# Optimization experiments

Hardware: AMD Instinct MI355X
Metric: run time of the kernel (lower is better)

## Reference

```python
import jax, jax.numpy as jnp
import numpy as np

B, TOPN, OUT, PAD, IOU_TH, IM = 16, 4, 224, 224, 0.25, 448
HP = IM + 2 * PAD  # padded image side = 896

_ANCHOR_SETTINGS = (
    dict(stride=32, size=48, scale=[2 ** (1. / 3.), 2 ** (2. / 3.)], aspect_ratio=[0.667, 1, 1.5]),
    dict(stride=64, size=96, scale=[2 ** (1. / 3.), 2 ** (2. / 3.)], aspect_ratio=[0.667, 1, 1.5]),
    dict(stride=128, size=192, scale=[1, 2 ** (1. / 3.), 2 ** (2. / 3.)], aspect_ratio=[0.667, 1, 1.5]),
)

def _edge_anchors(input_shape=(IM, IM)):
    # NTS-Net generate_default_anchor_maps: per layer, loop scale then aspect,
    # each emitting an HxW map flattened row-major -> matches tidy conv channel-major flatten.
    out = []
    for a in _ANCHOR_SETTINGS:
        st = a['stride']
        H = int(np.ceil(input_shape[0] / st)); W = int(np.ceil(input_shape[1] / st))
        cy = np.broadcast_to((np.arange(H) * st + st / 2.)[:, None], (H, W))
        cx = np.broadcast_to((np.arange(W) * st + st / 2.)[None, :], (H, W))
        for sc in a['scale']:
            for ar in a['aspect_ratio']:
                h = a['size'] * sc / np.sqrt(ar); w = a['size'] * sc * np.sqrt(ar)
                out.append(np.stack([cy - h / 2., cx - w / 2., cy + h / 2., cx + w / 2.], -1).reshape(-1, 4))
    e = np.concatenate(out, 0)
    return (e + PAD).astype(np.int32)  # module does (edge_anchors + 224).astype(int)


def _conv(x, w, b, stride, pad):
    y = jax.lax.conv_general_dilated(x, w, (stride, stride), [(pad, pad), (pad, pad)],
                                     dimension_numbers=('NCHW', 'OIHW', 'NCHW'))
    return y + b[None, :, None, None]


def _proposal_scores(rpn, w1, b1, w2, b2, w3, b3, wt1, bt1, wt2, bt2, wt3, bt3):
    d1 = jax.nn.relu(_conv(rpn, w1, b1, 1, 1))   # [B,128,14,14]
    d2 = jax.nn.relu(_conv(d1, w2, b2, 2, 1))    # [B,128,7,7]
    d3 = jax.nn.relu(_conv(d2, w3, b3, 2, 1))    # [B,128,4,4]
    bsz = rpn.shape[0]
    t1 = _conv(d1, wt1, bt1, 1, 0).reshape(bsz, -1)  # [B,1176]
    t2 = _conv(d2, wt2, bt2, 1, 0).reshape(bsz, -1)  # [B,294]
    t3 = _conv(d3, wt3, bt3, 1, 0).reshape(bsz, -1)  # [B,144]
    return jnp.concatenate([t1, t2, t3], axis=1)     # [B,1614]


def _nms_topn(scores, boxes, areas):
    # greedy hard NMS, fixed TOPN picks, suppress iou >= IOU_TH (matches upstream hard_nms)
    def step(s, _):
        i = jnp.argmax(s)
        sb = boxes[i]
        iy = jnp.clip(jnp.minimum(boxes[:, 2], sb[2]) - jnp.maximum(boxes[:, 0], sb[0]), 0.)
        ix = jnp.clip(jnp.minimum(boxes[:, 3], sb[3]) - jnp.maximum(boxes[:, 1], sb[1]), 0.)
        inter = iy * ix
        iou = inter / (areas + areas[i] - inter)
        return jnp.where(iou >= IOU_TH, -jnp.inf, s), i
    _, idxs = jax.lax.scan(step, scores, None, length=TOPN)
    return idxs  # [TOPN] int


def _crop_resize(x, anchors, top_idx):
    # batched replacement of the per-(i,j) F.interpolate(x_pad[i,:,y0:y1,x0:x1], 224, bilinear, align_corners=True)
    x_pad = jnp.pad(x, ((0, 0), (0, 0), (PAD, PAD), (PAD, PAD)))
    xp = jnp.transpose(x_pad, (0, 2, 3, 1))            # [B,HP,HP,3]
    bxs = anchors[top_idx].astype(jnp.float32)          # [B,T,4] (y0,x0,y1,x1)
    y0, x0, y1, x1 = bxs[..., 0], bxs[..., 1], bxs[..., 2], bxs[..., 3]
    t = jnp.arange(OUT, dtype=jnp.float32) / (OUT - 1)  # align_corners=True grid
    ys = y0[..., None] + t * (y1 - y0 - 1.)[..., None]  # [B,T,S] src rows in padded img
    xs = x0[..., None] + t * (x1 - x0 - 1.)[..., None]
    yi0 = jnp.floor(ys).astype(jnp.int32); yi1 = jnp.minimum(yi0 + 1, HP - 1)
    xi0 = jnp.floor(xs).astype(jnp.int32); xi1 = jnp.minimum(xi0 + 1, HP - 1)
    wy = (ys - yi0)[..., :, None, None]                 # [B,T,S,1,1]
    wx = (xs - xi0)[..., None, :, None]                 # [B,T,1,S,1]
    b = jnp.arange(x.shape[0])[:, None, None, None]
    g = lambda yi, xi: xp[b, yi[..., :, None], xi[..., None, :]]  # [B,T,S,S,3]
    v = (g(yi0, xi0) * (1 - wy) * (1 - wx) + g(yi0, xi1) * (1 - wy) * wx
         + g(yi1, xi0) * wy * (1 - wx) + g(yi1, xi1) * wy * wx)
    return jnp.transpose(v, (0, 1, 4, 2, 3))            # [B,T,3,S,S]


def setup_inputs() -> dict:
    key = jax.random.key(0)
    ks = jax.random.split(key, 16)
    he = lambda k, shape, fan: jax.random.normal(k, shape, jnp.float32) * np.sqrt(2.0 / fan)
    inp = {
        'x': jax.random.normal(ks[0], (B, 3, IM, IM), jnp.float32),
        'rpn_feature': jax.random.uniform(ks[1], (B, 2048, 14, 14), jnp.float32),
        'w_down1': he(ks[2], (128, 2048, 3, 3), 2048 * 9), 'b_down1': jnp.zeros((128,), jnp.float32),
        'w_down2': he(ks[3], (128, 128, 3, 3), 128 * 9),   'b_down2': jnp.zeros((128,), jnp.float32),
        'w_down3': he(ks[4], (128, 128, 3, 3), 128 * 9),   'b_down3': jnp.zeros((128,), jnp.float32),
        'w_tidy1': he(ks[5], (6, 128, 1, 1), 128),         'b_tidy1': jnp.zeros((6,), jnp.float32),
        'w_tidy2': he(ks[6], (6, 128, 1, 1), 128),         'b_tidy2': jnp.zeros((6,), jnp.float32),
        'w_tidy3': he(ks[7], (9, 128, 1, 1), 128),         'b_tidy3': jnp.zeros((9,), jnp.float32),
        'anchors': jnp.asarray(_edge_anchors(), jnp.int32),  # [1614,4]
    }
    return inp


def reference(x, rpn_feature, w_down1, b_down1, w_down2, b_down2, w_down3, b_down3,
              w_tidy1, b_tidy1, w_tidy2, b_tidy2, w_tidy3, b_tidy3, anchors):
    rpn_score = _proposal_scores(rpn_feature, w_down1, b_down1, w_down2, b_down2, w_down3, b_down3,
                                 w_tidy1, b_tidy1, w_tidy2, b_tidy2, w_tidy3, b_tidy3)
    boxes = anchors.astype(jnp.float32)
    areas = (boxes[:, 2] - boxes[:, 0]) * (boxes[:, 3] - boxes[:, 1])
    top_idx = jax.vmap(lambda s: _nms_topn(s, boxes, areas))(rpn_score)       # [B,TOPN]
    top_prob = jnp.take_along_axis(rpn_score, top_idx, axis=1)                # [B,TOPN]
    part_imgs = _crop_resize(x, anchors, top_idx).reshape(B * TOPN, 3, OUT, OUT)
    return part_imgs, top_idx, top_prob, rpn_score
```

## Files before the change

### kernel.cpp

```cpp
#include <hip/hip_runtime.h>
#include <math.h>

#define BATCH 16
#define TOPN 4
#define OUTS 224
#define PADW 224
#define IM 448
#define HP 896
#define NA 1614
#define IC1 2048
#define C128 128

#define N_PART (BATCH*TOPN*3*OUTS*OUTS)
#define OFF_TOPIDX  (N_PART)
#define OFF_TOPPROB (N_PART + BATCH*TOPN)
#define OFF_SCORE   (N_PART + 2*BATCH*TOPN)

#define WS_D1 0
#define WS_IDX (BATCH*C128*196)
#define WS_WT  (WS_IDX + 64)
#define NWT1 (9*2048*128)
#define NWT2 (9*128*128)
#define NIMG (16*32*16384)
#define D1SL 25088

typedef __attribute__((ext_vector_type(8))) short frag8;
typedef __attribute__((ext_vector_type(16))) float acc16;
typedef __attribute__((ext_vector_type(4)))  float acc4;

__device__ __forceinline__ unsigned short f2bf(float f) {
    unsigned int u = __float_as_uint(f);
    u = (u + 0x7fffu + ((u >> 16) & 1u)) >> 16;
    return (unsigned short)u;
}
__device__ __forceinline__ float bf2f(unsigned short h) {
    return __uint_as_float(((unsigned int)h) << 16);
}
__device__ __forceinline__ void cvt4(const float* v, ushort4* h, ushort4* lo) {
    unsigned short hh[4], ll[4];
#pragma unroll
    for (int e = 0; e < 4; ++e) { hh[e] = f2bf(v[e]); ll[e] = f2bf(v[e] - bf2f(hh[e])); }
    *h  = make_ushort4(hh[0], hh[1], hh[2], hh[3]);
    *lo = make_ushort4(ll[0], ll[1], ll[2], ll[3]);
}

__device__ __forceinline__ void w1frag_body(const float* __restrict__ w1,
                                            unsigned short* __restrict__ w1h,
                                            unsigned short* __restrict__ w1l,
                                            int i) {
    if (i >= 32768) return;
    int oc5 = i & 31;
    int q8  = (i >> 5) & 1;
    int ot  = (i >> 6) & 3;
    int c   = (i >> 8) & 3;
    int h   = (i >> 10) & 1;
    int kg  = (i >> 11) & 15;
    int oc  = ot * 32 + oc5;
    int ic0 = kg * 128 + h * 64 + c * 16 + q8 * 8;
    int l   = q8 * 32 + oc5;
    const float* src = w1 + ((size_t)oc * IC1 + ic0) * 9;
    size_t dbase = (size_t)kg * 16384 + h * 8192 + c * 2048 + ot * 512 + l * 8;
#pragma unroll
    for (int t = 0; t < 9; ++t) {
        frag8 hv, lv;
#pragma unroll
        for (int e = 0; e < 8; ++e) {
            float v = src[e * 9 + t];
            unsigned short hs = f2bf(v);
            hv[e] = (short)hs;
            lv[e] = (short)f2bf(v - bf2f(hs));
        }
        size_t dst = dbase + (size_t)t * 262144;
        *(frag8*)&w1h[dst] = hv;
        *(frag8*)&w1l[dst] = lv;
    }
}

__device__ __forceinline__ void wfrag128_body(const float* __restrict__ w,
                                              unsigned short* __restrict__ wh,
                                              unsigned short* __restrict__ wl,
                                              int i) {
    if (i >= 16384) return;
    int oc5 = i & 31;
    int q8  = (i >> 5) & 1;
    int ot  = (i >> 6) & 3;
    int c   = (i >> 8) & 3;
    int h   = (i >> 10) & 1;
    int oc  = ot * 32 + oc5;
    int ic0 = h * 64 + c * 16 + q8 * 8;
    int l   = q8 * 32 + oc5;
    const float* src = w + ((size_t)oc * C128 + ic0) * 9;
    size_t dbase = (size_t)h * 8192 + c * 2048 + ot * 512 + l * 8;
#pragma unroll
    for (int t = 0; t < 9; ++t) {
        frag8 hv, lv;
#pragma unroll
        for (int e = 0; e < 8; ++e) {
            float v = src[e * 9 + t];
            unsigned short hs = f2bf(v);
            hv[e] = (short)hs;
            lv[e] = (short)f2bf(v - bf2f(hs));
        }
        size_t dst = dbase + (size_t)t * 16384;
        *(frag8*)&wh[dst] = hv;
        *(frag8*)&wl[dst] = lv;
    }
}

__global__ __launch_bounds__(256) void k_prep(
    const float* __restrict__ w1, unsigned short* __restrict__ w1h, unsigned short* __restrict__ w1l,
    const float* __restrict__ w2, unsigned short* __restrict__ w2fh, unsigned short* __restrict__ w2fl,
    const float* __restrict__ w3, unsigned short* __restrict__ w3fh, unsigned short* __restrict__ w3fl,
    const float* __restrict__ rpn, unsigned short* __restrict__ imgH) {
    __shared__ float tile[64 * 201];
    const int tid = threadIdx.x;
    const int blk = blockIdx.x;
    if (blk < 128) {
        w1frag_body(w1, w1h, w1l, blk * 256 + tid);
    } else if (blk < 192) {
        wfrag128_body(w2, w2fh, w2fl, (blk - 128) * 256 + tid);
    } else if (blk < 256) {
        wfrag128_body(w3, w3fh, w3fl, (blk - 192) * 256 + tid);
    } else {
        const int bb = blk - 256;
        const int b = bb & 15, icg = bb >> 4;
        const int ic0 = icg * 64;
        char* img = (char*)(imgH + (size_t)bb * 16384);
        for (int qq = tid; qq < 3136; qq += 256) {
            int icl = qq / 49, r = qq % 49, p = r * 4;
            const float4 v = *(const float4*)&rpn[(size_t)(b * IC1 + ic0 + icl) * 196 + p];
            tile[icl * 201 + p + 0] = v.x;
            tile[icl * 201 + p + 1] = v.y;
            tile[icl * 201 + p + 2] = v.z;
            tile[icl * 201 + p + 3] = v.w;
        }
        __syncthreads();
        for (int qq = tid; qq < 3136; qq += 256) {
            int px = qq >> 4, ic4 = (qq & 15) * 4;
            float vv[4];
            unsigned short hh[4];
#pragma unroll
            for (int e = 0; e < 4; ++e) { vv[e] = tile[(ic4 + e) * 201 + px]; hh[e] = f2bf(vv[e]); }
            int pos = (px / 14 + 1) * 16 + (px % 14 + 1);
            int byo = (pos * 128 + ic4 * 2) ^ ((pos & 7) << 4);
            *(ushort4*)(img + byo) = make_ushort4(hh[0], hh[1], hh[2], hh[3]);
        }
        for (int qq = tid; qq < 960; qq += 256) {
            int hp = qq >> 4, sub = qq & 15;
            int pos;
            if (hp < 16)      pos = hp;
            else if (hp < 32) pos = 240 + (hp - 16);
            else if (hp < 46) pos = (hp - 31) * 16;
            else              pos = (hp - 45) * 16 + 15;
            *(ushort4*)(img + pos * 128 + sub * 8) = make_ushort4(0, 0, 0, 0);
        }
    }
}

#define LOADB(it, BH, BL) { \
    const int o_ = ((it) >> 2) * 262144 + ((it) & 3) * 2048; \
    BH = *(const frag8*)&WHb[o_]; BL = *(const frag8*)&WLb[o_]; }

#define DOMFMA(it, BH, BL) { \
    const int tap_ = (it) >> 2; \
    const int off_ = (tap_ / 3) * 16 + (tap_ % 3); \
    const int kb_ = ((it) & 3) * 32 + q * 16; \
    frag8 aH[4]; \
    _Pragma("unroll") \
    for (int mt_ = 0; mt_ < 4; ++mt_) { \
        const int p_ = posa[mt_] + off_; \
        const int by_ = (p_ * 128 + kb_) ^ ((p_ & 7) << 4); \
        aH[mt_] = *(const frag8*)((const char*)inH + by_); \
    } \
    _Pragma("unroll") \
    for (int mt_ = 0; mt_ < 4; ++mt_) { \
        acc[mt_] = __builtin_amdgcn_mfma_f32_32x32x16_bf16(aH[mt_], BH, acc[mt_], 0, 0, 0); \
        acc[mt_] = __builtin_amdgcn_mfma_f32_32x32x16_bf16(aH[mt_], BL, acc[mt_], 0, 0, 0); \
    } }

__global__ __launch_bounds__(512, 4) void k_conv1_mfma(const unsigned short* __restrict__ imgH,
                                                       const unsigned short* __restrict__ wfh,
                                                       const unsigned short* __restrict__ wfl,
                                                       float* __restrict__ d1p) {
    __shared__ unsigned short inH[256 * 64];

    const int tid = threadIdx.x;
    const int blk = blockIdx.x;
    const int b = blk >> 5;
    const int icg = blk & 31;
    const int l = tid & 63, w = tid >> 6;
    const int ln = l & 31, q = l >> 5;
    const int mtw = w & 1, ntw = w >> 1;

    {
        const char* src = (const char*)(imgH + ((size_t)(icg * 16 + b)) * 16384);
        char* dst = (char*)inH;
#pragma unroll
        for (int k = 0; k < 4; ++k) {
            frag8 v = *(const frag8*)(src + tid * 16 + k * 8192);
            *(frag8*)(dst + tid * 16 + k * 8192) = v;
        }
    }

    acc16 acc[4];
#pragma unroll
    for (int mt = 0; mt < 4; ++mt)
#pragma unroll
        for (int r = 0; r < 16; ++r) acc[mt][r] = 0.f;

    int posa[4];
#pragma unroll
    for (int mt = 0; mt < 4; ++mt) {
        int px = mtw * 128 + mt * 32 + ln;
        posa[mt] = (px < 196) ? ((px / 14) * 16 + (px % 14)) : 0;
    }

    const unsigned short* WHb = wfh + (size_t)icg * 8192 + ntw * 512 + (size_t)l * 8;
    const unsigned short* WLb = wfl + (size_t)icg * 8192 + ntw * 512 + (size_t)l * 8;

    __syncthreads();

    frag8 B0H, B0L, B1H, B1L, B2H, B2L;
    LOADB(0, B0H, B0L);
    LOADB(1, B1H, B1L);
    LOADB(2, B2H, B2L);
#pragma unroll
    for (int g = 0; g < 12; ++g) {
        DOMFMA(g * 3 + 0, B0H, B0L); if (g < 11) LOADB(g * 3 + 3, B0H, B0L);
        DOMFMA(g * 3 + 1, B1H, B1L); if (g < 11) LOADB(g * 3 + 4, B1H, B1L);
        DOMFMA(g * 3 + 2, B2H, B2L); if (g < 11) LOADB(g * 3 + 5, B2H, B2L);
    }

    {
        float* out = d1p + (size_t)blk * D1SL;
        const int oc = ntw * 32 + ln;
#pragma unroll
        for (int mt = 0; mt < 4; ++mt) {
#pragma unroll
            for (int r = 0; r < 16; ++r) {
                int m = (r & 3) + 8 * (r >> 2) + 4 * q;
                int px = mtw * 128 + mt * 32 + m;
                if (px < 196)
                    out[px * 128 + oc] = acc[mt][r];
            }
        }
    }
}

__global__ __launch_bounds__(256) void k_reduce(const float* __restrict__ d1p,
                                                const float* __restrict__ b1,
                                                float* __restrict__ d1) {
    int f4 = blockIdx.x * 256 + threadIdx.x;
    int flat = f4 * 4;
    int b = flat / D1SL;
    int inner = flat - b * D1SL;
    const float* src = d1p + (size_t)b * 32 * D1SL + inner;
    float4 s = *(const float4*)&b1[inner & 127];
#pragma unroll 8
    for (int icg = 0; icg < 32; ++icg) {
        float4 v = *(const float4*)&src[(size_t)icg * D1SL];
        s.x += v.x; s.y += v.y; s.z += v.z; s.w += v.w;
    }
    s.x = fmaxf(s.x, 0.f); s.y = fmaxf(s.y, 0.f);
    s.z = fmaxf(s.z, 0.f); s.w = fmaxf(s.w, 0.f);
    *(float4*)&d1[flat] = s;
}

__global__ __launch_bounds__(256, 1) void k_conv2t1(
    const float* __restrict__ d1,
    const unsigned short* __restrict__ w2fh, const unsigned short* __restrict__ w2fl,
    const float* __restrict__ b2,
    const float* __restrict__ wt1, const float* __restrict__ bt1,
    float* __restrict__ d2, float* __restrict__ score_out) {
    __shared__ unsigned short inH[304 * 72];
    __shared__ unsigned short inL[304 * 72];
    __shared__ unsigned short t1H[16 * 72];
    __shared__ unsigned short t1L[16 * 72];
    __shared__ float red[3 * 64 * 16];

    const int tid = threadIdx.x;
    const int blk = blockIdx.x;
    const int b = blk >> 3;
    const int pt = (blk >> 2) & 1;
    const int ot = blk & 3;
    const int l = tid & 63, w = tid >> 6;
    const int ln = l & 31, q = l >> 5;
    const int l16 = l & 15, q4 = l >> 4;

    acc16 c2;
    acc4 t1a[2];
#pragma unroll
    for (int r = 0; r < 16; ++r) c2[r] = 0.f;
#pragma unroll
    for (int i = 0; i < 2; ++i)
#pragma unroll
        for (int r = 0; r < 4; ++r) t1a[i][r] = 0.f;

    int posa2;
    {
        int px = pt * 32 + ln;
        posa2 = (px < 49) ? ((px / 7) * 32 + (px % 7) * 2) : 256;
    }
    const int ko = w * 16 + q * 8;

    for (int i = tid; i < 304 * 72; i += 256) { inH[i] = 0; inL[i] = 0; }
    __syncthreads();

    for (int half = 0; half < 2; ++half) {
        const int ics = half * 64;
        for (int qq = tid; qq < 3136; qq += 256) {
            int px = qq >> 4, ic4 = (qq & 15) * 4;
            float4 v = *(const float4*)&d1[(size_t)(b * 196 + px) * 128 + ics + ic4];
            float vv[4] = {fmaxf(v.x, 0.f), fmaxf(v.y, 0.f), fmaxf(v.z, 0.f), fmaxf(v.w, 0.f)};
            ushort4 h4, l4; cvt4(vv, &h4, &l4);
            int pos = (px / 14 + 1) * 16 + (px % 14 + 1);
            *(ushort4*)&inH[pos * 72 + ic4] = h4;
            *(ushort4*)&inL[pos * 72 + ic4] = l4;
        }
        if (ot == 0) {
            for (int qq = tid; qq < 1024; qq += 256) {
                int m = qq >> 6, k = qq & 63;
                float v = (m < 6) ? wt1[m * 128 + ics + k] : 0.f;
                unsigned short h = f2bf(v);
                t1H[m * 72 + k] = h;
                t1L[m * 72 + k] = f2bf(v - bf2f(h));
            }
        }
        __syncthreads();

        {
            const unsigned short* W2B  = w2fh + half * 8192 + w * 2048 + ot * 512 + (size_t)l * 8;
            const unsigned short* W2Bl = w2fl + half * 8192 + w * 2048 + ot * 512 + (size_t)l * 8;
            frag8 B0H = *(const frag8*)&W2B[0],     B0L = *(const frag8*)&W2Bl[0];
            frag8 B1H = *(const frag8*)&W2B[16384], B1L = *(const frag8*)&W2Bl[16384];
#pragma unroll
            for (int j = 0; j < 9; ++j) {
                const int off = (j / 3) * 16 + (j % 3);
                const int pp = (posa2 + off) * 72 + ko;
                frag8 aH = *(const frag8*)&inH[pp];
                frag8 aL = *(const frag8*)&inL[pp];
                frag8 BH = (j & 1) ? B1H : B0H;
                frag8 BL = (j & 1) ? B1L : B0L;
                c2 = __builtin_amdgcn_mfma_f32_32x32x16_bf16(aH, BH, c2, 0, 0, 0);
                c2 = __builtin_amdgcn_mfma_f32_32x32x16_bf16(aH, BL, c2, 0, 0, 0);
                c2 = __builtin_amdgcn_mfma_f32_32x32x16_bf16(aL, BH, c2, 0, 0, 0);
                if (j < 7) {
                    if (j & 1) { B1H = *(const frag8*)&W2B[(j + 2) * 16384]; B1L = *(const frag8*)&W2Bl[(j + 2) * 16384]; }
                    else       { B0H = *(const frag8*)&W2B[(j + 2) * 16384]; B0L = *(const frag8*)&W2Bl[(j + 2) * 16384]; }
                }
            }
        }

        if (ot == 0) {
#pragma unroll
            for (int i = 0; i < 2; ++i) {
                int px = (pt * 8 + w * 2 + i) * 16 + l16;
                int pos = (px < 196) ? ((px / 14 + 1) * 16 + (px % 14 + 1)) : 256;
#pragma unroll
                for (int c = 0; c < 2; ++c) {
                    int kot = c * 32 + q4 * 8;
                    frag8 aH = *(const frag8*)&t1H[l16 * 72 + kot];
                    frag8 aL = *(const frag8*)&t1L[l16 * 72 + kot];
                    frag8 bH = *(const frag8*)&inH[pos * 72 + kot];
                    frag8 bL = *(const frag8*)&inL[pos * 72 + kot];
                    t1a[i] = __builtin_amdgcn_mfma_f32_16x16x32_bf16(aH, bH, t1a[i], 0, 0, 0);
                    t1a[i] = __builtin_amdgcn_mfma_f32_16x16x32_bf16(aH, bL, t1a[i], 0, 0, 0);
                    t1a[i] = __builtin_amdgcn_mfma_f32_16x16x32_bf16(aL, bH, t1a[i], 0, 0, 0);
                }
            }
        }
        __syncthreads();
    }

    if (w > 0) {
#pragma unroll
        for (int r = 0; r < 16; ++r) red[((w - 1) * 64 + l) * 16 + r] = c2[r];
    }
    __syncthreads();
    if (w == 0) {
        const int oc = ot * 32 + ln;
        float bias = b2[oc];
#pragma unroll
        for (int r = 0; r < 16; ++r) {
            float s = c2[r] + red[(0 * 64 + l) * 16 + r] + red[(1 * 64 + l) * 16 + r] + red[(2 * 64 + l) * 16 + r];
            int m = (r & 3) + 8 * (r >> 2) + 4 * q;
            int px = pt * 32 + m;
            if (px < 49) d2[(size_t)(b * 49 + px) * 128 + oc] = fmaxf(s + bias, 0.f);
        }
    }
    if (ot == 0) {
#pragma unroll
        for (int i = 0; i < 2; ++i) {
            int px = (pt * 8 + w * 2 + i) * 16 + l16;
#pragma unroll
            for (int r = 0; r < 4; ++r) {
                int oc = q4 * 4 + r;
                if (oc < 6 && px < 196)
                    score_out[b * NA + oc * 196 + px] = t1a[i][r] + bt1[oc];
            }
        }
    }
}

__global__ __launch_bounds__(256, 1) void k_conv3t2(
    const float* __restrict__ d2,
    const unsigned short* __restrict__ w3fh, const unsigned short* __restrict__ w3fl,
    const float* __restrict__ b3,
    const float* __restrict__ wt2, const float* __restrict__ bt2,
    float* __restrict__ d3, float* __restrict__ score_out) {
    __shared__ unsigned short dhH[192 * 72];
    __shared__ unsigned short dhL[192 * 72];
    __shared__ unsigned short t2H[16 * 72];
    __shared__ unsigned short t2L[16 * 72];
    __shared__ float red[3 * 64 * 16];

    const int tid = threadIdx.x;
    const int blk = blockIdx.x;
    const int b = blk >> 2;
    const int ot = blk & 3;
    const int l = tid & 63, w = tid >> 6;
    const int ln = l & 31, q = l >> 5;
    const int l16 = l & 15, q4 = l >> 4;

    acc16 c3;
    acc4 t2a;
#pragma unroll
    for (int r = 0; r < 16; ++r) c3[r] = 0.f;
#pragma unroll
    for (int r = 0; r < 4; ++r) t2a[r] = 0.f;

    const int posb3 = (ln < 16) ? ((ln / 4) * 32 + (ln % 4) * 2) : 144;
    const int pxt2 = w * 16 + l16;
    const int posbt2 = (pxt2 < 49) ? ((pxt2 / 7 + 1) * 16 + (pxt2 % 7 + 1)) : 144;
    const int ko = w * 16 + q * 8;

    for (int i = tid; i < 192 * 72; i += 256) { dhH[i] = 0; dhL[i] = 0; }
    __syncthreads();

    for (int half = 0; half < 2; ++half) {
        const int ics = half * 64;
        for (int qq = tid; qq < 784; qq += 256) {
            int px = qq >> 4, ic4 = (qq & 15) * 4;
            float4 v = *(const float4*)&d2[(size_t)(b * 49 + px) * 128 + ics + ic4];
            float vv[4] = {v.x, v.y, v.z, v.w};
            ushort4 h4, l4; cvt4(vv, &h4, &l4);
            int pos = (px / 7 + 1) * 16 + (px % 7 + 1);
            *(ushort4*)&dhH[pos * 72 + ic4] = h4;
            *(ushort4*)&dhL[pos * 72 + ic4] = l4;
        }
        if (ot == 0) {
            for (int qq = tid; qq < 1024; qq += 256) {
                int m = qq >> 6, k = qq & 63;
                float v = (m < 6) ? wt2[m * 128 + ics + k] : 0.f;
                unsigned short h = f2bf(v);
                t2H[m * 72 + k] = h;
                t2L[m * 72 + k] = f2bf(v - bf2f(h));
            }
        }
        __syncthreads();

        {
            const unsigned short* W3B  = w3fh + half * 8192 + w * 2048 + ot * 512 + (size_t)l * 8;
            const unsigned short* W3Bl = w3fl + half * 8192 + w * 2048 + ot * 512 + (size_t)l * 8;
            frag8 B0H = *(const frag8*)&W3B[0],     B0L = *(const frag8*)&W3Bl[0];
            frag8 B1H = *(const frag8*)&W3B[16384], B1L = *(const frag8*)&W3Bl[16384];
#pragma unroll
            for (int j = 0; j < 9; ++j) {
                const int off = (j / 3) * 16 + (j % 3);
                const int pp = (posb3 + off) * 72 + ko;
                frag8 aH = *(const frag8*)&dhH[pp];
                frag8 aL = *(const frag8*)&dhL[pp];
                frag8 BH = (j & 1) ? B1H : B0H;
                frag8 BL = (j & 1) ? B1L : B0L;
                c3 = __builtin_amdgcn_mfma_f32_32x32x16_bf16(aH, BH, c3, 0, 0, 0);
                c3 = __builtin_amdgcn_mfma_f32_32x32x16_bf16(aH, BL, c3, 0, 0, 0);
                c3 = __builtin_amdgcn_mfma_f32_32x32x16_bf16(aL, BH, c3, 0, 0, 0);
                if (j < 7) {
                    if (j & 1) { B1H = *(const frag8*)&W3B[(j + 2) * 16384]; B1L = *(const frag8*)&W3Bl[(j + 2) * 16384]; }
                    else       { B0H = *(const frag8*)&W3B[(j + 2) * 16384]; B0L = *(const frag8*)&W3Bl[(j + 2) * 16384]; }
                }
            }
        }

        if (ot == 0) {
#pragma unroll
            for (int c = 0; c < 2; ++c) {
                int kot = c * 32 + q4 * 8;
                frag8 aH = *(const frag8*)&t2H[l16 * 72 + kot];
                frag8 aL = *(const frag8*)&t2L[l16 * 72 + kot];
                frag8 bH = *(const frag8*)&dhH[posbt2 * 72 + kot];
                frag8 bL = *(const frag8*)&dhL[posbt2 * 72 + kot];
                t2a = __builtin_amdgcn_mfma_f32_16x16x32_bf16(aH, bH, t2a, 0, 0, 0);
                t2a = __builtin_amdgcn_mfma_f32_16x16x32_bf16(aH, bL, t2a, 0, 0, 0);
                t2a = __builtin_amdgcn_mfma_f32_16x16x32_bf16(aL, bH, t2a, 0, 0, 0);
            }
        }
        __syncthreads();
    }

    if (w > 0) {
#pragma unroll
        for (int r = 0; r < 16; ++r) red[((w - 1) * 64 + l) * 16 + r] = c3[r];
    }
    __syncthreads();
    if (w == 0) {
        const int oc = ot * 32 + ln;
        float bias = b3[oc];
#pragma unroll
        for (int r = 0; r < 16; ++r) {
            float s = c3[r] + red[(0 * 64 + l) * 16 + r] + red[(1 * 64 + l) * 16 + r] + red[(2 * 64 + l) * 16 + r];
            int px = (r & 3) + 8 * (r >> 2) + 4 * q;
            if (px < 16) d3[(size_t)(b * 128 + oc) * 16 + px] = fmaxf(s + bias, 0.f);
        }
    }
    if (ot == 0) {
#pragma unroll
        for (int r = 0; r < 4; ++r) {
            int oc = q4 * 4 + r;
            if (oc < 6 && pxt2 < 49)
                score_out[b * NA + 1176 + oc * 49 + pxt2] = t2a[r] + bt2[oc];
        }
    }
}

__global__ __launch_bounds__(512, 1) void k_t3nms(
    const float* __restrict__ d3, const float* __restrict__ wt3, const float* __restrict__ bt3,
    const int* __restrict__ anchors, float* __restrict__ score_out,
    float* __restrict__ out_idx, float* __restrict__ out_prob, int* __restrict__ idx_ws) {
    __shared__ float wt3s[1152];
    __shared__ float d3s[2048];
    __shared__ float sbuf[NA];
    __shared__ float y0s[NA], x0s[NA], y1s[NA], x1s[NA], ars[NA];
    __shared__ float rv[8];
    __shared__ int ri[9];

    const int tid = threadIdx.x;
    const int b = blockIdx.x;
    const int l = tid & 63, w = tid >> 6;

    for (int i = tid; i < 1152; i += 512) wt3s[i] = wt3[i];
    for (int i = tid; i < 2048; i += 512) d3s[i] = d3[b * 2048 + i];
    for (int j = tid; j < 1470; j += 512) sbuf[j] = score_out[b * NA + j];
    for (int j = tid; j < NA; j += 512) {
        int4 a = ((const int4*)anchors)[j];
        float a0 = (float)a.x, a1 = (float)a.y, a2 = (float)a.z, a3 = (float)a.w;
        y0s[j] = a0; x0s[j] = a1; y1s[j] = a2; x1s[j] = a3;
        ars[j] = (a2 - a0) * (a3 - a1);
    }
    __syncthreads();

    if (tid < 144) {
        int oc = tid >> 4, px = tid & 15;
        float s = bt3[oc];
        for (int ic = 0; ic < 128; ++ic) s += wt3s[oc * 128 + ic] * d3s[ic * 16 + px];
        sbuf[1470 + oc * 16 + px] = s;
        score_out[b * NA + 1470 + oc * 16 + px] = s;
    }
    __syncthreads();

    for (int it = 0; it < TOPN; ++it) {
        float bv = -INFINITY; int bi = NA;
        for (int j = tid; j < NA; j += 512) {
            float v = sbuf[j];
            if (v > bv || (v == bv && j < bi)) { bv = v; bi = j; }
        }
#pragma unroll
        for (int d = 1; d < 64; d <<= 1) {
            float ov = __shfl_xor(bv, d, 64);
            int   oi = __shfl_xor(bi, d, 64);
            if (ov > bv || (ov == bv && oi < bi)) { bv = ov; bi = oi; }
        }
        if (l == 0) { rv[w] = bv; ri[w] = bi; }
        __syncthreads();
        if (tid == 0) {
            float V = rv[0]; int K = ri[0];
#pragma unroll
            for (int j = 1; j < 8; ++j) {
                float ov = rv[j]; int oi = ri[j];
                if (ov > V || (ov == V && oi < K)) { V = ov; K = oi; }
            }
            ri[8] = K;
            out_idx[b * TOPN + it] = (float)K;
            out_prob[b * TOPN + it] = V;
            idx_ws[b * TOPN + it] = K;
        }
        __syncthreads();
        int K = ri[8];
        float ky0 = y0s[K], kx0 = x0s[K], ky1 = y1s[K], kx1 = x1s[K], ka = ars[K];
        for (int j = tid; j < NA; j += 512) {
            float iy = fmaxf(fminf(y1s[j], ky1) - fmaxf(y0s[j], ky0), 0.f);
            float ix = fmaxf(fminf(x1s[j], kx1) - fmaxf(x0s[j], kx0), 0.f);
            float inter = iy * ix;
            float iou = inter / (ars[j] + ka - inter);
            if (iou >= 0.25f) sbuf[j] = -INFINITY;
        }
        __syncthreads();
    }
}

__global__ __launch_bounds__(256) void k_crop(const float* __restrict__ x,
                                              const int* __restrict__ anchors,
                                              const int* __restrict__ idx_ws,
                                              float* __restrict__ out) {
    int blk = blockIdx.x;
    int crop = blk / OUTS;
    int i = blk % OUTS;
    int j = threadIdx.x;
    if (j >= OUTS) return;
    int b = crop >> 2;
    int a = idx_ws[crop];
    int y0 = anchors[a * 4], x0 = anchors[a * 4 + 1];
    int y1 = anchors[a * 4 + 2], x1 = anchors[a * 4 + 3];

    float ti = (float)i / 223.f;
    float ys = (float)y0 + ti * (float)(y1 - y0 - 1);
    int yi0 = (int)ys;
    int yi1 = min(yi0 + 1, HP - 1);
    float wy = ys - (float)yi0;

    float tj = (float)j / 223.f;
    float xs = (float)x0 + tj * (float)(x1 - x0 - 1);
    int xi0 = (int)xs;
    int xi1 = min(xi0 + 1, HP - 1);
    float wx = xs - (float)xi0;

    int ry0 = yi0 - PADW, ry1 = yi1 - PADW, rx0 = xi0 - PADW, rx1 = xi1 - PADW;
    bool vy0 = (ry0 >= 0) && (ry0 < IM), vy1 = (ry1 >= 0) && (ry1 < IM);
    bool vx0 = (rx0 >= 0) && (rx0 < IM), vx1 = (rx1 >= 0) && (rx1 < IM);

    float w00 = (1.f - wy) * (1.f - wx), w01 = (1.f - wy) * wx;
    float w10 = wy * (1.f - wx), w11 = wy * wx;

#pragma unroll
    for (int c = 0; c < 3; ++c) {
        const float* xp = x + (size_t)(b * 3 + c) * IM * IM;
        float g00 = (vy0 && vx0) ? xp[ry0 * IM + rx0] : 0.f;
        float g01 = (vy0 && vx1) ? xp[ry0 * IM + rx1] : 0.f;
        float g10 = (vy1 && vx0) ? xp[ry1 * IM + rx0] : 0.f;
        float g11 = (vy1 && vx1) ? xp[ry1 * IM + rx1] : 0.f;
        out[(size_t)(crop * 3 + c) * OUTS * OUTS + i * OUTS + j] =
            g00 * w00 + g01 * w01 + g10 * w10 + g11 * w11;
    }
}

extern "C" void kernel_launch(void* const* d_in, const int* in_sizes, int n_in,
                              void* d_out, int out_size, void* d_ws, size_t ws_size,
                              hipStream_t stream) {
    (void)in_sizes; (void)n_in; (void)out_size; (void)ws_size;
    const float* x    = (const float*)d_in[0];
    const float* rpn  = (const float*)d_in[1];
    const float* w1   = (const float*)d_in[2];
    const float* b1   = (const float*)d_in[3];
    const float* w2   = (const float*)d_in[4];
    const float* b2   = (const float*)d_in[5];
    const float* w3   = (const float*)d_in[6];
    const float* b3   = (const float*)d_in[7];
    const float* wt1  = (const float*)d_in[8];
    const float* bt1  = (const float*)d_in[9];
    const float* wt2  = (const float*)d_in[10];
    const float* bt2  = (const float*)d_in[11];
    const float* wt3  = (const float*)d_in[12];
    const float* bt3  = (const float*)d_in[13];
    const int*   anc  = (const int*)d_in[14];

    float* out = (float*)d_out;
    float* ws  = (float*)d_ws;
    float* d1  = ws + WS_D1;
    int*   idxw = (int*)(ws + WS_IDX);
    unsigned short* w1h = (unsigned short*)(ws + WS_WT);
    unsigned short* w1l = w1h + NWT1;
    unsigned short* w2fh = w1l + NWT1;
    unsigned short* w2fl = w2fh + NWT2;
    unsigned short* w3fh = w2fl + NWT2;
    unsigned short* w3fl = w3fh + NWT2;
    unsigned short* imgH = w3fl + NWT2;
    float* d1p = (float*)(imgH + NIMG);
    float* d2  = d1p + (size_t)512 * D1SL;
    float* d3  = d2 + 16 * 49 * 128;

    k_prep<<<768, 256, 0, stream>>>(w1, w1h, w1l, w2, w2fh, w2fl, w3, w3fh, w3fl,
                                    rpn, imgH);
    k_conv1_mfma<<<512, 512, 0, stream>>>(imgH, w1h, w1l, d1p);
    k_reduce<<<392, 256, 0, stream>>>(d1p, b1, d1);
    k_conv2t1<<<128, 256, 0, stream>>>(d1, w2fh, w2fl, b2, wt1, bt1,
                                       d2, out + OFF_SCORE);
    k_conv3t2<<<64, 256, 0, stream>>>(d2, w3fh, w3fl, b3, wt2, bt2,
                                      d3, out + OFF_SCORE);
    k_t3nms<<<BATCH, 512, 0, stream>>>(d3, wt3, bt3, anc, out + OFF_SCORE,
                                       out + OFF_TOPIDX, out + OFF_TOPPROB, idxw);
    k_crop<<<BATCH * TOPN * OUTS, 256, 0, stream>>>(x, anc, idxw, out);
}
```

Measured before the change: 257.6 us.

## Fuse conv3/tidy2 kernel with tidy3+NMS kernel into one per-batch block

Merges the conv3+tidy2 kernel (64 blocks of 256 threads) and the tidy3+NMS kernel into a single kernel with one 512-thread block per image. Dynamic shared memory is reused between phases, and d3 stays in LDS instead of going through global memory. The intent is to drop one kernel launch and the d3 global round trip. In exchange, the conv3 work for each image runs on 8 waves in one block instead of 16 waves spread over 4 blocks, so parallelism falls from 64 to 16 blocks.

```diff
diff --git a/kernel.cpp b/kernel.cpp
--- a/kernel.cpp
+++ b/kernel.cpp
@@ -402,26 +402,42 @@
     }
 }
 
-__global__ __launch_bounds__(256, 1) void k_conv3t2(
+#define TAIL2_LDS 84480
+
+__global__ __launch_bounds__(512, 1) void k_tail2(
     const float* __restrict__ d2,
     const unsigned short* __restrict__ w3fh, const unsigned short* __restrict__ w3fl,
     const float* __restrict__ b3,
     const float* __restrict__ wt2, const float* __restrict__ bt2,
-    float* __restrict__ d3, float* __restrict__ score_out) {
-    __shared__ unsigned short dhH[192 * 72];
-    __shared__ unsigned short dhL[192 * 72];
-    __shared__ unsigned short t2H[16 * 72];
-    __shared__ unsigned short t2L[16 * 72];
-    __shared__ float red[3 * 64 * 16];
+    const float* __restrict__ wt3, const float* __restrict__ bt3,
+    const int* __restrict__ anchors, float* __restrict__ score_out,
+    float* __restrict__ out_idx, float* __restrict__ out_prob, int* __restrict__ idx_ws) {
+    extern __shared__ char smem[];
+    unsigned short* dhH = (unsigned short*)(smem);
+    unsigned short* dhL = (unsigned short*)(smem + 27648);
+    unsigned short* t2H = (unsigned short*)(smem + 55296);
+    unsigned short* t2L = (unsigned short*)(smem + 57600);
+    float* red  = (float*)(smem + 59904);
+    float* d3s  = (float*)(smem + 76288);
+    float* wt3s = (float*)(smem);
+    float* sbuf = (float*)(smem + 4608);
+    float* y0s  = (float*)(smem + 11064);
+    float* x0s  = (float*)(smem + 17520);
+    float* y1s  = (float*)(smem + 23976);
+    float* x1s  = (float*)(smem + 30432);
+    float* ars  = (float*)(smem + 36888);
+    float* rv   = (float*)(smem + 43344);
+    int*   ri   = (int*)(smem + 43376);
 
     const int tid = threadIdx.x;
-    const int blk = blockIdx.x;
-    const int b = blk >> 2;
-    const int ot = blk & 3;
+    const int b = blockIdx.x;
     const int l = tid & 63, w = tid >> 6;
     const int ln = l & 31, q = l >> 5;
     const int l16 = l & 15, q4 = l >> 4;
 
+    const int ot = w & 3;
+    const int ks = w >> 2;
+
     acc16 c3;
     acc4 t2a;
 #pragma unroll
@@ -431,15 +447,14 @@
 
     const int posb3 = (ln < 16) ? ((ln / 4) * 32 + (ln % 4) * 2) : 144;
     const int pxt2 = w * 16 + l16;
-    const int posbt2 = (pxt2 < 49) ? ((pxt2 / 7 + 1) * 16 + (pxt2 % 7 + 1)) : 144;
-    const int ko = w * 16 + q * 8;
-
-    for (int i = tid; i < 192 * 72; i += 256) { dhH[i] = 0; dhL[i] = 0; }
+    const int posbt2 = (w < 4 && pxt2 < 49) ? ((pxt2 / 7 + 1) * 16 + (pxt2 % 7 + 1)) : 144;
+
+    for (int i = tid; i < 192 * 72; i += 512) { dhH[i] = 0; dhL[i] = 0; }
     __syncthreads();
 
     for (int half = 0; half < 2; ++half) {
         const int ics = half * 64;
-        for (int qq = tid; qq < 784; qq += 256) {
+        for (int qq = tid; qq < 784; qq += 512) {
             int px = qq >> 4, ic4 = (qq & 15) * 4;
             float4 v = *(const float4*)&d2[(size_t)(b * 49 + px) * 128 + ics + ic4];
             float vv[4] = {v.x, v.y, v.z, v.w};
@@ -448,20 +463,21 @@
             *(ushort4*)&dhH[pos * 72 + ic4] = h4;
             *(ushort4*)&dhL[pos * 72 + ic4] = l4;
         }
-        if (ot == 0) {
-            for (int qq = tid; qq < 1024; qq += 256) {
-                int m = qq >> 6, k = qq & 63;
-                float v = (m < 6) ? wt2[m * 128 + ics + k] : 0.f;
-                unsigned short h = f2bf(v);
-                t2H[m * 72 + k] = h;
-                t2L[m * 72 + k] = f2bf(v - bf2f(h));
-            }
-        }
-        __syncthreads();
-
-        {
-            const unsigned short* W3B  = w3fh + half * 8192 + w * 2048 + ot * 512 + (size_t)l * 8;
-            const unsigned short* W3Bl = w3fl + half * 8192 + w * 2048 + ot * 512 + (size_t)l * 8;
+        for (int qq = tid; qq < 1024; qq += 512) {
+            int m = qq >> 6, k = qq & 63;
+            float v = (m < 6) ? wt2[m * 128 + ics + k] : 0.f;
+            unsigned short h = f2bf(v);
+            t2H[m * 72 + k] = h;
+            t2L[m * 72 + k] = f2bf(v - bf2f(h));
+        }
+        __syncthreads();
+
+#pragma unroll
+        for (int ci = 0; ci < 2; ++ci) {
+            const int c = ks * 2 + ci;
+            const int ko = c * 16 + q * 8;
+            const unsigned short* W3B  = w3fh + half * 8192 + c * 2048 + ot * 512 + (size_t)l * 8;
+            const unsigned short* W3Bl = w3fl + half * 8192 + c * 2048 + ot * 512 + (size_t)l * 8;
             frag8 B0H = *(const frag8*)&W3B[0],     B0L = *(const frag8*)&W3Bl[0];
             frag8 B1H = *(const frag8*)&W3B[16384], B1L = *(const frag8*)&W3Bl[16384];
 #pragma unroll
@@ -482,7 +498,7 @@
             }
         }
 
-        if (ot == 0) {
+        if (w < 4) {
 #pragma unroll
             for (int c = 0; c < 2; ++c) {
                 int kot = c * 32 + q4 * 8;
@@ -498,49 +514,34 @@
         __syncthreads();
     }
 
-    if (w > 0) {
-#pragma unroll
-        for (int r = 0; r < 16; ++r) red[((w - 1) * 64 + l) * 16 + r] = c3[r];
-    }
-    __syncthreads();
-    if (w == 0) {
+    if (w >= 4) {
+#pragma unroll
+        for (int r = 0; r < 16; ++r) red[((w - 4) * 64 + l) * 16 + r] = c3[r];
+    }
+    __syncthreads();
+    if (w < 4) {
         const int oc = ot * 32 + ln;
         float bias = b3[oc];
 #pragma unroll
         for (int r = 0; r < 16; ++r) {
-            float s = c3[r] + red[(0 * 64 + l) * 16 + r] + red[(1 * 64 + l) * 16 + r] + red[(2 * 64 + l) * 16 + r];
+            float s = c3[r] + red[(w * 64 + l) * 16 + r];
             int px = (r & 3) + 8 * (r >> 2) + 4 * q;
-            if (px < 16) d3[(size_t)(b * 128 + oc) * 16 + px] = fmaxf(s + bias, 0.f);
-        }
-    }
-    if (ot == 0) {
+            if (px < 16) d3s[oc * 16 + px] = fmaxf(s + bias, 0.f);
+        }
 #pragma unroll
         for (int r = 0; r < 4; ++r) {
-            int oc = q4 * 4 + r;
-            if (oc < 6 && pxt2 < 49)
-                score_out[b * NA + 1176 + oc * 49 + pxt2] = t2a[r] + bt2[oc];
-        }
-    }
-}
-
-__global__ __launch_bounds__(512, 1) void k_t3nms(
-    const float* __restrict__ d3, const float* __restrict__ wt3, const float* __restrict__ bt3,
-    const int* __restrict__ anchors, float* __restrict__ score_out,
-    float* __restrict__ out_idx, float* __restrict__ out_prob, int* __restrict__ idx_ws) {
-    __shared__ float wt3s[1152];
-    __shared__ float d3s[2048];
-    __shared__ float sbuf[NA];
-    __shared__ float y0s[NA], x0s[NA], y1s[NA], x1s[NA], ars[NA];
-    __shared__ float rv[8];
-    __shared__ int ri[9];
-
-    const int tid = threadIdx.x;
-    const int b = blockIdx.x;
-    const int l = tid & 63, w = tid >> 6;
+            int oc2 = q4 * 4 + r;
+            if (oc2 < 6 && pxt2 < 49) {
+                float v = t2a[r] + bt2[oc2];
+                sbuf[1176 + oc2 * 49 + pxt2] = v;
+                score_out[b * NA + 1176 + oc2 * 49 + pxt2] = v;
+            }
+        }
+    }
+    __syncthreads();
 
     for (int i = tid; i < 1152; i += 512) wt3s[i] = wt3[i];
-    for (int i = tid; i < 2048; i += 512) d3s[i] = d3[b * 2048 + i];
-    for (int j = tid; j < 1470; j += 512) sbuf[j] = score_out[b * NA + j];
+    for (int j = tid; j < 1176; j += 512) sbuf[j] = score_out[b * NA + j];
     for (int j = tid; j < NA; j += 512) {
         int4 a = ((const int4*)anchors)[j];
         float a0 = (float)a.x, a1 = (float)a.y, a2 = (float)a.z, a3 = (float)a.w;
@@ -676,7 +677,8 @@
     unsigned short* imgH = w3fl + NWT2;
     float* d1p = (float*)(imgH + NIMG);
     float* d2  = d1p + (size_t)512 * D1SL;
-    float* d3  = d2 + 16 * 49 * 128;
+
+    hipFuncSetAttribute((const void*)k_tail2, hipFuncAttributeMaxDynamicSharedMemorySize, TAIL2_LDS);
 
     k_prep<<<768, 256, 0, stream>>>(w1, w1h, w1l, w2, w2fh, w2fl, w3, w3fh, w3fl,
                                     rpn, imgH);
@@ -684,9 +686,8 @@
     k_reduce<<<392, 256, 0, stream>>>(d1p, b1, d1);
     k_conv2t1<<<128, 256, 0, stream>>>(d1, w2fh, w2fl, b2, wt1, bt1,
                                        d2, out + OFF_SCORE);
-    k_conv3t2<<<64, 256, 0, stream>>>(d2, w3fh, w3fl, b3, wt2, bt2,
-                                      d3, out + OFF_SCORE);
-    k_t3nms<<<BATCH, 512, 0, stream>>>(d3, wt3, bt3, anc, out + OFF_SCORE,
-                                       out + OFF_TOPIDX, out + OFF_TOPPROB, idxw);
+    k_tail2<<<BATCH, 512, TAIL2_LDS, stream>>>(d2, w3fh, w3fl, b3, wt2, bt2,
+                                               wt3, bt3, anc, out + OFF_SCORE,
+                                               out + OFF_TOPIDX, out + OFF_TOPPROB, idxw);
     k_crop<<<BATCH * TOPN * OUTS, 256, 0, stream>>>(x, anc, idxw, out);
 }
```

After: 261.3 us. Within noise of the previous version (+1.4%).
